# Kernel tuning notes

Measured on AMD Instinct MI355X. Metric: run time of the kernel, lower is better.

The kernel has to match this reference:

```python
import jax, jax.numpy as jnp
import numpy as np
import math

HEAD_SIZE = 64
N_EMBED = 1024
BLOCK_SIZE = 2048
BATCH = 8


def setup_inputs() -> dict:
    key = jax.random.key(0)
    k1, k2, k3, k4, k5 = jax.random.split(key, 5)
    index = jax.random.normal(k1, (BATCH, BLOCK_SIZE, N_EMBED), dtype=jnp.float32)
    memory = jax.random.normal(k2, (BATCH, BLOCK_SIZE, N_EMBED), dtype=jnp.float32)
    # torch Linear weights: [out_features, in_features], kaiming-uniform-ish init
    bound = 1.0 / math.sqrt(N_EMBED)
    Wq = jax.random.uniform(k3, (HEAD_SIZE, N_EMBED), jnp.float32, -bound, bound)
    Wk = jax.random.uniform(k4, (HEAD_SIZE, N_EMBED), jnp.float32, -bound, bound)
    Wv = jax.random.uniform(k5, (HEAD_SIZE, N_EMBED), jnp.float32, -bound, bound)
    return {"index": index, "memory": memory, "Wq": Wq, "Wk": Wk, "Wv": Wv}


def reference(index, memory, Wq, Wk, Wv):
    # q/k/v projections (Linear without bias: x @ W.T)
    q = jnp.einsum('btc,hc->bth', index, Wq)   # [B,T,H]
    k = jnp.einsum('bsc,hc->bsh', memory, Wk)  # [B,S,H]
    v = jnp.einsum('bsc,hc->bsh', memory, Wv)  # [B,S,H]
    scale = 1.0 / math.sqrt(HEAD_SIZE)
    w = jnp.einsum('bth,bsh->bts', q, k) * scale  # [B,T,S]
    # causal mask: tril==0 -> -inf
    T = index.shape[1]
    causal = jnp.tril(jnp.ones((BLOCK_SIZE, BLOCK_SIZE), dtype=bool))[:T, :T]
    w = jnp.where(causal, w, -jnp.inf)
    w = jax.nn.softmax(w, axis=-1)
    out = jnp.einsum('bts,bsh->bth', w, v)  # [B,T,H]
    return out
```

## Files before the change

kernel.cpp:

```cpp
#include <hip/hip_runtime.h>
#include <math.h>

typedef __bf16 bf16;
typedef __bf16 bf16x4 __attribute__((ext_vector_type(4)));
typedef __bf16 bf16x8 __attribute__((ext_vector_type(8)));
typedef float f32x4 __attribute__((ext_vector_type(4)));

#define MFMA16(a,b,c) __builtin_amdgcn_mfma_f32_16x16x32_bf16((a),(b),(c),0,0,0)

static constexpr int HS  = 64;
static constexpr int SEQ = 2048;
static constexpr int NE  = 1024;
static constexpr int NB  = 8;

__device__ __forceinline__ bf16x8 cvt8(float4 a, float4 b) {
  bf16x8 r;
  r[0]=(bf16)a.x; r[1]=(bf16)a.y; r[2]=(bf16)a.z; r[3]=(bf16)a.w;
  r[4]=(bf16)b.x; r[5]=(bf16)b.y; r[6]=(bf16)b.z; r[7]=(bf16)b.w;
  return r;
}

__device__ __forceinline__ void gload16(const void* g, void* l) {
  __builtin_amdgcn_global_load_lds(
      (const __attribute__((address_space(1))) void*)g,
      (__attribute__((address_space(3))) void*)l, 16, 0, 0);
}

__global__ __launch_bounds__(256) void wcvt_kernel(
    const float* __restrict__ Wq, const float* __restrict__ Wk,
    const float* __restrict__ Wv, bf16* __restrict__ wqb,
    bf16* __restrict__ wkb, bf16* __restrict__ wvb)
{
  int i = (blockIdx.x * 256 + threadIdx.x) * 4;
  float4 q = *(const float4*)(Wq + i);
  float4 k = *(const float4*)(Wk + i);
  float4 v = *(const float4*)(Wv + i);
  bf16x4 qo, ko, vo;
  qo[0]=(bf16)(q.x*0.125f); qo[1]=(bf16)(q.y*0.125f); qo[2]=(bf16)(q.z*0.125f); qo[3]=(bf16)(q.w*0.125f);
  ko[0]=(bf16)k.x; ko[1]=(bf16)k.y; ko[2]=(bf16)k.z; ko[3]=(bf16)k.w;
  vo[0]=(bf16)v.x; vo[1]=(bf16)v.y; vo[2]=(bf16)v.z; vo[3]=(bf16)v.w;
  *(bf16x4*)(wqb + i) = qo;
  *(bf16x4*)(wkb + i) = ko;
  *(bf16x4*)(wvb + i) = vo;
}

template<int KV>
__device__ __forceinline__ void proj_body(
    const float* __restrict__ X, const bf16* __restrict__ W0,
    const bf16* __restrict__ W1, bf16* __restrict__ out0,
    bf16* __restrict__ outVT, int slab, char* smem)
{
  const int tid  = threadIdx.x;
  const int lane = tid & 63;
  const int w    = tid >> 6;
  const int m    = lane & 15;
  const int g    = lane >> 4;
  const int rowBase = slab * 64;

  char* Xb  = smem;
  char* W0b = smem + 49152;
  char* W1b = smem + 73728;

  const f32x4 vz = {0.f,0.f,0.f,0.f};
  f32x4 accA[4] = {vz, vz, vz, vz};
  f32x4 accB[4] = {vz, vz, vz, vz};

  const float* Xbase = X + (size_t)rowBase * NE;

  auto stage = [&](int kt, int buf) {
#pragma unroll
    for (int q = 0; q < 4; ++q) {
      int r = (q*4 + w)*4 + (lane >> 4);
      int s = lane & 15;
      const float* src = Xbase + (size_t)r * NE + kt*64 + ((s ^ (r & 15)) * 4);
      void* dst = Xb + buf*16384 + (q*4 + w)*1024;
      gload16(src, dst);
    }
#pragma unroll
    for (int q = 0; q < 2; ++q) {
      int r = (q*4 + w)*8 + (lane >> 3);
      int s = lane & 7;
      size_t soff = (size_t)r * NE + kt*64 + ((s ^ (r & 7)) * 8);
      void* dst0 = W0b + buf*8192 + (q*4 + w)*1024;
      gload16(W0 + soff, dst0);
      if (KV) {
        void* dst1 = W1b + buf*8192 + (q*4 + w)*1024;
        gload16(W1 + soff, dst1);
      }
    }
  };

  auto compute = [&](int buf) {
#pragma unroll
    for (int kk = 0; kk < 2; ++kk) {
      const int arow = 16*w + m;
      const int s0 = 2*(kk*4 + g);
      const char* ab = Xb + buf*16384 + arow*256;
      float4 x0 = *(const float4*)(ab + (( s0      ^ (arow & 15)) * 16));
      float4 x1 = *(const float4*)(ab + (((s0 + 1) ^ (arow & 15)) * 16));
      bf16x8 af = cvt8(x0, x1);
#pragma unroll
      for (int n = 0; n < 4; ++n) {
        const int col = 16*n + m;
        const int ws  = kk*4 + g;
        bf16x8 b0 = *(const bf16x8*)(W0b + buf*8192 + col*128 + ((ws ^ (col & 7)) * 16));
        accA[n] = MFMA16(af, b0, accA[n]);
        if (KV) {
          bf16x8 b1 = *(const bf16x8*)(W1b + buf*8192 + col*128 + ((ws ^ (col & 7)) * 16));
          accB[n] = MFMA16(af, b1, accB[n]);
        }
      }
    }
  };

  stage(0, 0);
  stage(1, 1);
#pragma unroll
  for (int t = 0; t < 16; ++t) {
    if (t < 15) {
      if (KV) asm volatile("s_waitcnt vmcnt(8)" ::: "memory");
      else    asm volatile("s_waitcnt vmcnt(6)" ::: "memory");
    } else {
      asm volatile("s_waitcnt vmcnt(0)" ::: "memory");
    }
    __builtin_amdgcn_s_barrier();
    __builtin_amdgcn_sched_barrier(0);
    if (t + 2 < 16) stage(t + 2, (t + 2) % 3);
    __builtin_amdgcn_sched_barrier(0);
    compute(t % 3);
  }

#pragma unroll
  for (int n = 0; n < 4; ++n)
#pragma unroll
    for (int i = 0; i < 4; ++i) {
      int row = rowBase + 16*w + 4*g + i;
      int h   = 16*n + m;
      out0[(size_t)row * HS + h] = (bf16)accA[n][i];
      if (KV)
        outVT[((size_t)(row >> 11) * HS + h) * SEQ + (row & 2047)] =
            (bf16)accB[n][i];
    }
}

__global__ __launch_bounds__(256, 2) void proj_kernel(
    const float* __restrict__ index, const float* __restrict__ memory,
    const bf16* __restrict__ wqb, const bf16* __restrict__ wkb,
    const bf16* __restrict__ wvb, bf16* __restrict__ qb,
    bf16* __restrict__ kb, bf16* __restrict__ vtb)
{
  __shared__ __align__(1024) char smem[98304];
  if (blockIdx.x < 256)
    proj_body<0>(index,  wqb, nullptr, qb, nullptr, blockIdx.x, smem);
  else
    proj_body<1>(memory, wkb, wvb,     kb, vtb, blockIdx.x - 256, smem);
}

__global__ __launch_bounds__(128) void attn_kernel(
    const bf16* __restrict__ qb, const bf16* __restrict__ kb,
    const bf16* __restrict__ vtb, float* __restrict__ out)
{
  __shared__ __align__(16) bf16 Ks[2][64][72];
  __shared__ __align__(16) bf16 VTs[2][64][72];
  __shared__ __align__(16) bf16 Ps[2][16][72];

  const int tid  = threadIdx.x;
  const int lane = tid & 63;
  const int w    = tid >> 6;
  const int m    = lane & 15;
  const int g    = lane >> 4;
  const int qt   = 127 - blockIdx.x;
  const int b    = blockIdx.y;
  const int nkv  = (qt >> 2) + 1;
  const int r0   = lane >> 1;
  const int hh   = (lane & 1) * 32;

  bf16x8 qf0 = *(const bf16x8*)(qb + ((size_t)b*SEQ + qt*16 + m)*HS + g*8);
  bf16x8 qf1 = *(const bf16x8*)(qb + ((size_t)b*SEQ + qt*16 + m)*HS + 32 + g*8);

  const f32x4 vz = {0.f,0.f,0.f,0.f};
  f32x4 o_acc[4] = {vz, vz, vz, vz};
  float mrun = -INFINITY, lrun = 0.f;

  bf16x8 kp[8], vp[8];
  const bf16* kbB = kb  + (size_t)b*SEQ*HS;
  const bf16* vtB = vtb + (size_t)b*HS*SEQ;

  auto loadKV = [&](int j) {
    const bf16* kt_ = kbB + (size_t)j*64*HS;
    const bf16* vt_ = vtB + j*64;
#pragma unroll
    for (int q = 0; q < 4; ++q) {
      kp[q]   = *(const bf16x8*)(kt_ + (size_t)r0*64        + hh + q*8);
      kp[4+q] = *(const bf16x8*)(kt_ + (size_t)(r0+32)*64   + hh + q*8);
      vp[q]   = *(const bf16x8*)(vt_ + (size_t)r0*SEQ       + hh + q*8);
      vp[4+q] = *(const bf16x8*)(vt_ + (size_t)(r0+32)*SEQ  + hh + q*8);
    }
  };
  auto writeKV = [&]() {
#pragma unroll
    for (int q = 0; q < 4; ++q) {
      *(bf16x8*)&Ks[w][r0][hh + q*8]      = kp[q];
      *(bf16x8*)&Ks[w][r0+32][hh + q*8]   = kp[4+q];
      *(bf16x8*)&VTs[w][r0][hh + q*8]     = vp[q];
      *(bf16x8*)&VTs[w][r0+32][hh + q*8]  = vp[4+q];
    }
  };

  int j = w;
  if (j < nkv) {
    loadKV(j);
    writeKV();
    while (true) {
      const int jn = j + 2;
      const bool more = jn < nkv;
      if (more) loadKV(jn);

      f32x4 s_acc[4];
#pragma unroll
      for (int na = 0; na < 4; ++na) {
        f32x4 z = vz;
        z = MFMA16(*(const bf16x8*)&Ks[w][16*na + m][g*8],      qf0, z);
        z = MFMA16(*(const bf16x8*)&Ks[w][16*na + m][32 + g*8], qf1, z);
        s_acc[na] = z;
      }
      if (j == nkv - 1) {
        const int q_ = qt*16 + m;
#pragma unroll
        for (int na = 0; na < 4; ++na)
#pragma unroll
          for (int i = 0; i < 4; ++i)
            if (j*64 + 16*na + 4*g + i > q_) s_acc[na][i] = -INFINITY;
      }

      float mx = fmaxf(
        fmaxf(fmaxf(fmaxf(s_acc[0][0],s_acc[0][1]),fmaxf(s_acc[0][2],s_acc[0][3])),
              fmaxf(fmaxf(s_acc[1][0],s_acc[1][1]),fmaxf(s_acc[1][2],s_acc[1][3]))),
        fmaxf(fmaxf(fmaxf(s_acc[2][0],s_acc[2][1]),fmaxf(s_acc[2][2],s_acc[2][3])),
              fmaxf(fmaxf(s_acc[3][0],s_acc[3][1]),fmaxf(s_acc[3][2],s_acc[3][3]))));
      mx = fmaxf(mx, __shfl_xor(mx, 16));
      mx = fmaxf(mx, __shfl_xor(mx, 32));
      float mnew = fmaxf(mrun, mx);
      float corr = __expf(mrun - mnew);
      mrun = mnew;
      float ts = 0.f;
#pragma unroll
      for (int na = 0; na < 4; ++na) {
        bf16x4 pk;
#pragma unroll
        for (int i = 0; i < 4; ++i) {
          float p = __expf(s_acc[na][i] - mnew);
          ts += p;
          pk[i] = (bf16)p;
        }
        *(bf16x4*)&Ps[w][m][16*na + 4*g] = pk;
      }
      ts += __shfl_xor(ts, 16);
      ts += __shfl_xor(ts, 32);
      lrun = lrun * corr + ts;
#pragma unroll
      for (int nd = 0; nd < 4; ++nd)
#pragma unroll
        for (int i = 0; i < 4; ++i) o_acc[nd][i] *= corr;

      bf16x8 pf0 = *(const bf16x8*)&Ps[w][m][g*8];
      bf16x8 pf1 = *(const bf16x8*)&Ps[w][m][32 + g*8];
#pragma unroll
      for (int nd = 0; nd < 4; ++nd) {
        o_acc[nd] = MFMA16(*(const bf16x8*)&VTs[w][16*nd + m][g*8],      pf0, o_acc[nd]);
        o_acc[nd] = MFMA16(*(const bf16x8*)&VTs[w][16*nd + m][32 + g*8], pf1, o_acc[nd]);
      }

      if (!more) break;
      writeKV();
      j = jn;
    }
  }

  float* PO = (float*)&Ks[w][0][0];
  float* PM = (float*)&VTs[w][0][0];
#pragma unroll
  for (int nd = 0; nd < 4; ++nd)
    *(f32x4*)&PO[m*68 + 16*nd + 4*g] = o_acc[nd];
  if (g == 0) { PM[m] = mrun; PM[16 + m] = lrun; }
  __syncthreads();

  {
    const int r  = tid >> 3;
    const int c0 = (tid & 7) * 8;
    const float* O0 = (const float*)&Ks[0][0][0];
    const float* O1 = (const float*)&Ks[1][0][0];
    const float* M0 = (const float*)&VTs[0][0][0];
    const float* M1 = (const float*)&VTs[1][0][0];
    float m0 = M0[r], l0 = M0[16 + r];
    float m1 = M1[r], l1 = M1[16 + r];
    float mx = fmaxf(m0, m1);
    float s0 = __expf(m0 - mx), s1 = __expf(m1 - mx);
    float inv = 1.f / (s0*l0 + s1*l1);
    float4 x0 = *(const float4*)(O0 + r*68 + c0);
    float4 x1 = *(const float4*)(O0 + r*68 + c0 + 4);
    float4 y0 = *(const float4*)(O1 + r*68 + c0);
    float4 y1 = *(const float4*)(O1 + r*68 + c0 + 4);
    float4 o0, o1;
    o0.x=(x0.x*s0+y0.x*s1)*inv; o0.y=(x0.y*s0+y0.y*s1)*inv;
    o0.z=(x0.z*s0+y0.z*s1)*inv; o0.w=(x0.w*s0+y0.w*s1)*inv;
    o1.x=(x1.x*s0+y1.x*s1)*inv; o1.y=(x1.y*s0+y1.y*s1)*inv;
    o1.z=(x1.z*s0+y1.z*s1)*inv; o1.w=(x1.w*s0+y1.w*s1)*inv;
    float* op = out + ((size_t)b*SEQ + qt*16 + r) * HS + c0;
    *(float4*)(op)     = o0;
    *(float4*)(op + 4) = o1;
  }
}

extern "C" void kernel_launch(void* const* d_in, const int* in_sizes, int n_in,
                              void* d_out, int out_size, void* d_ws, size_t ws_size,
                              hipStream_t stream) {
  (void)in_sizes; (void)n_in; (void)out_size; (void)ws_size;
  const float* index  = (const float*)d_in[0];
  const float* memory = (const float*)d_in[1];
  const float* Wq     = (const float*)d_in[2];
  const float* Wk     = (const float*)d_in[3];
  const float* Wv     = (const float*)d_in[4];
  float* out = (float*)d_out;

  bf16* qb  = (bf16*)d_ws;
  bf16* kb  = qb  + (size_t)NB * SEQ * HS;
  bf16* vtb = kb  + (size_t)NB * SEQ * HS;
  bf16* wqb = vtb + (size_t)NB * SEQ * HS;
  bf16* wkb = wqb + (size_t)HS * NE;
  bf16* wvb = wkb + (size_t)HS * NE;

  wcvt_kernel<<<dim3(64), 256, 0, stream>>>(Wq, Wk, Wv, wqb, wkb, wvb);
  proj_kernel<<<dim3(512), 256, 0, stream>>>(index, memory, wqb, wkb, wvb, qb, kb, vtb);
  attn_kernel<<<dim3(128, 8), 128, 0, stream>>>(qb, kb, vtb, out);
}
```

Baseline: 72.37 us.

## Switch projection pipeline from triple to double LDS buffering

The projection kernel's shared-memory staging goes from three rotating buffers (96 KB) to two named buffers (64 KB). A second barrier after compute lets the next stage be issued into the buffer just consumed. Cutting LDS per block could allow more resident blocks per CU, and named buffers give simpler addressing. In exchange there is an extra barrier per iteration and less prefetch distance, so loads overlap compute less. The vmcnt wait counts were not changed for the new issue order.

```diff
diff --git a/kernel.cpp b/kernel.cpp
--- a/kernel.cpp
+++ b/kernel.cpp
@@ -48,7 +48,8 @@
 __device__ __forceinline__ void proj_body(
     const float* __restrict__ X, const bf16* __restrict__ W0,
     const bf16* __restrict__ W1, bf16* __restrict__ out0,
-    bf16* __restrict__ outVT, int slab, char* smem)
+    bf16* __restrict__ outVT, int slab,
+    char* Xs0, char* Xs1, char* W0s0, char* W0s1, char* W1s0, char* W1s1)
 {
   const int tid  = threadIdx.x;
   const int lane = tid & 63;
@@ -57,45 +58,36 @@
   const int g    = lane >> 4;
   const int rowBase = slab * 64;
 
-  char* Xb  = smem;
-  char* W0b = smem + 49152;
-  char* W1b = smem + 73728;
-
   const f32x4 vz = {0.f,0.f,0.f,0.f};
   f32x4 accA[4] = {vz, vz, vz, vz};
   f32x4 accB[4] = {vz, vz, vz, vz};
 
   const float* Xbase = X + (size_t)rowBase * NE;
 
-  auto stage = [&](int kt, int buf) {
+  auto stage = [&](int kt, char* Xd, char* W0d, char* W1d) {
 #pragma unroll
     for (int q = 0; q < 4; ++q) {
       int r = (q*4 + w)*4 + (lane >> 4);
       int s = lane & 15;
       const float* src = Xbase + (size_t)r * NE + kt*64 + ((s ^ (r & 15)) * 4);
-      void* dst = Xb + buf*16384 + (q*4 + w)*1024;
-      gload16(src, dst);
+      gload16(src, Xd + (q*4 + w)*1024);
     }
 #pragma unroll
     for (int q = 0; q < 2; ++q) {
       int r = (q*4 + w)*8 + (lane >> 3);
       int s = lane & 7;
       size_t soff = (size_t)r * NE + kt*64 + ((s ^ (r & 7)) * 8);
-      void* dst0 = W0b + buf*8192 + (q*4 + w)*1024;
-      gload16(W0 + soff, dst0);
-      if (KV) {
-        void* dst1 = W1b + buf*8192 + (q*4 + w)*1024;
-        gload16(W1 + soff, dst1);
-      }
+      gload16(W0 + soff, W0d + (q*4 + w)*1024);
+      if (KV) gload16(W1 + soff, W1d + (q*4 + w)*1024);
     }
   };
 
-  auto compute = [&](int buf) {
+  auto compute = [&](const char* Xd, const char* W0d, const char* W1d) {
 #pragma unroll
     for (int kk = 0; kk < 2; ++kk) {
       const int arow = 16*w + m;
       const int s0 = 2*(kk*4 + g);
-      const char* ab = Xb + buf*16384 + arow*256;
+      const char* ab = Xd + arow*256;
       float4 x0 = *(const float4*)(ab + (( s0      ^ (arow & 15)) * 16));
       float4 x1 = *(const float4*)(ab + (((s0 + 1) ^ (arow & 15)) * 16));
       bf16x8 af = cvt8(x0, x1);
@@ -103,18 +95,18 @@
       for (int n = 0; n < 4; ++n) {
         const int col = 16*n + m;
         const int ws  = kk*4 + g;
-        bf16x8 b0 = *(const bf16x8*)(W0b + buf*8192 + col*128 + ((ws ^ (col & 7)) * 16));
+        bf16x8 b0 = *(const bf16x8*)(W0d + col*128 + ((ws ^ (col & 7)) * 16));
         accA[n] = MFMA16(af, b0, accA[n]);
         if (KV) {
-          bf16x8 b1 = *(const bf16x8*)(W1b + buf*8192 + col*128 + ((ws ^ (col & 7)) * 16));
+          bf16x8 b1 = *(const bf16x8*)(W1d + col*128 + ((ws ^ (col & 7)) * 16));
           accB[n] = MFMA16(af, b1, accB[n]);
         }
       }
     }
   };
 
-  stage(0, 0);
-  stage(1, 1);
+  stage(0, Xs0, W0s0, W1s0);
+  stage(1, Xs1, W0s1, W1s1);
 #pragma unroll
   for (int t = 0; t < 16; ++t) {
     if (t < 15) {
@@ -125,9 +117,14 @@
     }
     __builtin_amdgcn_s_barrier();
     __builtin_amdgcn_sched_barrier(0);
-    if (t + 2 < 16) stage(t + 2, (t + 2) % 3);
+    if ((t & 1) == 0) compute(Xs0, W0s0, W1s0);
+    else              compute(Xs1, W0s1, W1s1);
     __builtin_amdgcn_sched_barrier(0);
-    compute(t % 3);
+    __builtin_amdgcn_s_barrier();
+    if (t + 2 < 16) {
+      if ((t & 1) == 0) stage(t + 2, Xs0, W0s0, W1s0);
+      else              stage(t + 2, Xs1, W0s1, W1s1);
+    }
   }
 
 #pragma unroll
@@ -149,11 +146,15 @@
     const bf16* __restrict__ wvb, bf16* __restrict__ qb,
     bf16* __restrict__ kb, bf16* __restrict__ vtb)
 {
-  __shared__ __align__(1024) char smem[98304];
+  __shared__ __align__(1024) char Xs0[16384], Xs1[16384];
+  __shared__ __align__(1024) char W0s0[8192], W0s1[8192];
+  __shared__ __align__(1024) char W1s0[8192], W1s1[8192];
   if (blockIdx.x < 256)
-    proj_body<0>(index,  wqb, nullptr, qb, nullptr, blockIdx.x, smem);
+    proj_body<0>(index,  wqb, nullptr, qb, nullptr, blockIdx.x,
+                 Xs0, Xs1, W0s0, W0s1, W1s0, W1s1);
   else
-    proj_body<1>(memory, wkb, wvb,     kb, vtb, blockIdx.x - 256, smem);
+    proj_body<1>(memory, wkb, wvb,     kb, vtb, blockIdx.x - 256,
+                 Xs0, Xs1, W0s0, W0s1, W1s0, W1s1);
 }
 
 __global__ __launch_bounds__(128) void attn_kernel(
```

Result: no change. 72.86 us (+0.7%).

## Split K and V projections into separate blocks with double-buffered LDS

Applied to the files above, without the earlier changes.

The projection kernel now gives Q, K and V each their own 256 blocks (768 total) instead of one block computing both K and V. The 3-stage global_load_lds pipeline with explicit vmcnt waits becomes a simpler 2-buffer loop with __syncthreads, which cuts LDS per block to 48KB and raises the occupancy hint to 3 blocks per CU. The catch is that the memory input is now read twice from HBM, once for K and once for V, and the pipeline is shallower, so it hides load latency less well.

```diff
diff --git a/kernel.cpp b/kernel.cpp
--- a/kernel.cpp
+++ b/kernel.cpp
@@ -44,11 +44,11 @@
   *(bf16x4*)(wvb + i) = vo;
 }
 
-template<int KV>
+template<int TRANS>
 __device__ __forceinline__ void proj_body(
-    const float* __restrict__ X, const bf16* __restrict__ W0,
-    const bf16* __restrict__ W1, bf16* __restrict__ out0,
-    bf16* __restrict__ outVT, int slab, char* smem)
+    const float* __restrict__ X, const bf16* __restrict__ W,
+    bf16* __restrict__ outN, bf16* __restrict__ outT, int slab,
+    char* Xb, char* Wb)
 {
   const int tid  = threadIdx.x;
   const int lane = tid & 63;
@@ -57,13 +57,8 @@
   const int g    = lane >> 4;
   const int rowBase = slab * 64;
 
-  char* Xb  = smem;
-  char* W0b = smem + 49152;
-  char* W1b = smem + 73728;
-
   const f32x4 vz = {0.f,0.f,0.f,0.f};
-  f32x4 accA[4] = {vz, vz, vz, vz};
-  f32x4 accB[4] = {vz, vz, vz, vz};
+  f32x4 acc[4] = {vz, vz, vz, vz};
 
   const float* Xbase = X + (size_t)rowBase * NE;
 
@@ -73,20 +68,14 @@
       int r = (q*4 + w)*4 + (lane >> 4);
       int s = lane & 15;
       const float* src = Xbase + (size_t)r * NE + kt*64 + ((s ^ (r & 15)) * 4);
-      void* dst = Xb + buf*16384 + (q*4 + w)*1024;
-      gload16(src, dst);
+      gload16(src, Xb + buf*16384 + (q*4 + w)*1024);
     }
 #pragma unroll
     for (int q = 0; q < 2; ++q) {
       int r = (q*4 + w)*8 + (lane >> 3);
       int s = lane & 7;
       size_t soff = (size_t)r * NE + kt*64 + ((s ^ (r & 7)) * 8);
-      void* dst0 = W0b + buf*8192 + (q*4 + w)*1024;
-      gload16(W0 + soff, dst0);
-      if (KV) {
-        void* dst1 = W1b + buf*8192 + (q*4 + w)*1024;
-        gload16(W1 + soff, dst1);
-      }
+      gload16(W + soff, Wb + buf*8192 + (q*4 + w)*1024);
     }
   };
 
@@ -103,31 +92,20 @@
       for (int n = 0; n < 4; ++n) {
         const int col = 16*n + m;
         const int ws  = kk*4 + g;
-        bf16x8 b0 = *(const bf16x8*)(W0b + buf*8192 + col*128 + ((ws ^ (col & 7)) * 16));
-        accA[n] = MFMA16(af, b0, accA[n]);
-        if (KV) {
-          bf16x8 b1 = *(const bf16x8*)(W1b + buf*8192 + col*128 + ((ws ^ (col & 7)) * 16));
-          accB[n] = MFMA16(af, b1, accB[n]);
-        }
+        bf16x8 b0 = *(const bf16x8*)(Wb + buf*8192 + col*128 + ((ws ^ (col & 7)) * 16));
+        acc[n] = MFMA16(af, b0, acc[n]);
       }
     }
   };
 
   stage(0, 0);
-  stage(1, 1);
-#pragma unroll
-  for (int t = 0; t < 16; ++t) {
-    if (t < 15) {
-      if (KV) asm volatile("s_waitcnt vmcnt(8)" ::: "memory");
-      else    asm volatile("s_waitcnt vmcnt(6)" ::: "memory");
-    } else {
-      asm volatile("s_waitcnt vmcnt(0)" ::: "memory");
-    }
-    __builtin_amdgcn_s_barrier();
-    __builtin_amdgcn_sched_barrier(0);
-    if (t + 2 < 16) stage(t + 2, (t + 2) % 3);
-    __builtin_amdgcn_sched_barrier(0);
-    compute(t % 3);
+  __syncthreads();
+  int buf = 0;
+  for (int kt = 0; kt < 16; ++kt) {
+    if (kt + 1 < 16) stage(kt + 1, buf ^ 1);
+    compute(buf);
+    __syncthreads();
+    buf ^= 1;
   }
 
 #pragma unroll
@@ -136,24 +114,29 @@
     for (int i = 0; i < 4; ++i) {
       int row = rowBase + 16*w + 4*g + i;
       int h   = 16*n + m;
-      out0[(size_t)row * HS + h] = (bf16)accA[n][i];
-      if (KV)
-        outVT[((size_t)(row >> 11) * HS + h) * SEQ + (row & 2047)] =
-            (bf16)accB[n][i];
-    }
-}
-
-__global__ __launch_bounds__(256, 2) void proj_kernel(
+      if (!TRANS)
+        outN[(size_t)row * HS + h] = (bf16)acc[n][i];
+      else
+        outT[((size_t)(row >> 11) * HS + h) * SEQ + (row & 2047)] =
+            (bf16)acc[n][i];
+    }
+}
+
+__global__ __launch_bounds__(256, 3) void proj_kernel(
     const float* __restrict__ index, const float* __restrict__ memory,
     const bf16* __restrict__ wqb, const bf16* __restrict__ wkb,
     const bf16* __restrict__ wvb, bf16* __restrict__ qb,
     bf16* __restrict__ kb, bf16* __restrict__ vtb)
 {
-  __shared__ __align__(1024) char smem[98304];
-  if (blockIdx.x < 256)
-    proj_body<0>(index,  wqb, nullptr, qb, nullptr, blockIdx.x, smem);
+  __shared__ __align__(1024) char Xb[32768];
+  __shared__ __align__(1024) char Wb[16384];
+  const int bid = blockIdx.x;
+  if (bid < 256)
+    proj_body<0>(index,  wqb, qb, nullptr, bid,       Xb, Wb);
+  else if (bid < 512)
+    proj_body<0>(memory, wkb, kb, nullptr, bid - 256, Xb, Wb);
   else
-    proj_body<1>(memory, wkb, wvb,     kb, vtb, blockIdx.x - 256, smem);
+    proj_body<1>(memory, wvb, nullptr, vtb, bid - 512, Xb, Wb);
 }
 
 __global__ __launch_bounds__(128) void attn_kernel(
@@ -331,6 +314,6 @@
   bf16* wvb = wkb + (size_t)HS * NE;
 
   wcvt_kernel<<<dim3(64), 256, 0, stream>>>(Wq, Wk, Wv, wqb, wkb, wvb);
-  proj_kernel<<<dim3(512), 256, 0, stream>>>(index, memory, wqb, wkb, wvb, qb, kb, vtb);
+  proj_kernel<<<dim3(768), 256, 0, stream>>>(index, memory, wqb, wkb, wvb, qb, kb, vtb);
   attn_kernel<<<dim3(128, 8), 128, 0, stream>>>(qb, kb, vtb, out);
 }
```

After: 72.38 us. No clear change (+0.0%).
